# Kernel optimization log

Hardware: AMD Instinct MI355X
Metric: run time of the kernel (lower is better)

Reference implementation:

```python
import jax, jax.numpy as jnp
import numpy as np

S, B, D = 2048, 32, 1024  # seq_len, batch, in_dim; out_dim = 2*D

def setup_inputs() -> dict:
    key = jax.random.key(0)
    k1, k2, k3, k4 = jax.random.split(key, 4)
    return {
        "input": jax.random.normal(k1, (S, B, D), dtype=jnp.float32),
        "h": jax.random.normal(k2, (B, D), dtype=jnp.float32),
        "Wi": jax.random.normal(k3, (D, D), dtype=jnp.float32) * 0.02,
        "Wo": jax.random.normal(k4, (D, 2 * D), dtype=jnp.float32) * 0.02,
    }

def reference(input, h, Wi, Wo):
    # semi = Wi(h), broadcast over seq dim (torch expand_as)
    semi = h @ Wi.T                                   # [B, D]
    # score logits: elementwise mult + sum over feature dim
    logits = jnp.einsum('sbd,bd->bs', input, semi)    # [B, S]
    # legacy nn.Softmax() on 2D tensor normalizes over dim=1 (= seq)
    attn = jax.nn.softmax(logits, axis=1)             # [B, S]
    # weighted sum over sequence
    s_tilde = jnp.einsum('bs,sbd->bd', attn, input)   # [B, D]
    # output projection + tanh
    c_t = jnp.tanh(jnp.concatenate([s_tilde, h], axis=1) @ Wo.T)  # [B, D]
    return c_t
```

## Files before the change

kernel.cpp:

```cpp
#include <hip/hip_runtime.h>
#include <math.h>

#define S_LEN    2048
#define BATCH    32
#define DIM      1024
#define P_CHUNKS 32
#define CHUNK    (S_LEN / P_CHUNKS)
#define ROWS_PER_WAVE (CHUNK / 4)
#define NPART    (P_CHUNKS * 4)

__global__ __launch_bounds__(256) void gemm_skinny(
    const float* __restrict__ A, const float* __restrict__ W,
    float* __restrict__ out, int K, int Dout, int act)
{
    __shared__ __align__(16) float At[2][32 * 256];

    const int t    = threadIdx.x;
    const int lane = t & 63;
    const int wid  = t >> 6;
    const int d    = blockIdx.x * 4 + wid;

    float acc[32];
#pragma unroll
    for (int b = 0; b < 32; ++b) acc[b] = 0.0f;

    float4 sreg[8];
#pragma unroll
    for (int i = 0; i < 8; ++i) {
        int f4id = t + i * 256;
        int bb   = f4id >> 6;
        int c4   = f4id & 63;
        sreg[i] = ((const float4*)(A + (size_t)bb * K))[c4];
    }
    float4 w4 = ((const float4*)(W + (size_t)d * K))[lane];

    int buf = 0;
    for (int k0 = 0; k0 < K; k0 += 256) {
#pragma unroll
        for (int i = 0; i < 8; ++i) {
            int f4id = t + i * 256;
            int bb   = f4id >> 6;
            int c4   = f4id & 63;
            ((float4*)At[buf])[bb * 64 + c4] = sreg[i];
        }
        __syncthreads();

        float4 w4c = w4;
        if (k0 + 256 < K) {
            const int k1 = k0 + 256;
#pragma unroll
            for (int i = 0; i < 8; ++i) {
                int f4id = t + i * 256;
                int bb   = f4id >> 6;
                int c4   = f4id & 63;
                sreg[i] = ((const float4*)(A + (size_t)bb * K + k1))[c4];
            }
            w4 = ((const float4*)(W + (size_t)d * K + k1))[lane];
        }

#pragma unroll
        for (int b = 0; b < 32; ++b) {
            float4 a4 = ((const float4*)At[buf])[b * 64 + lane];
            acc[b] = fmaf(w4c.x, a4.x, acc[b]);
            acc[b] = fmaf(w4c.y, a4.y, acc[b]);
            acc[b] = fmaf(w4c.z, a4.z, acc[b]);
            acc[b] = fmaf(w4c.w, a4.w, acc[b]);
        }
        buf ^= 1;
    }

    float mine = 0.0f;
#pragma unroll
    for (int b = 0; b < 32; ++b) {
        float v = acc[b];
#pragma unroll
        for (int off = 32; off > 0; off >>= 1) v += __shfl_xor(v, off, 64);
        if (lane == b) mine = v;
    }
    if (lane < 32) {
        float o = act ? tanhf(mine) : mine;
        out[(size_t)lane * Dout + d] = o;
    }
}

__global__ __launch_bounds__(256) void attn_partial(
    const float* __restrict__ input, const float* __restrict__ semi,
    float* __restrict__ pacc, float* __restrict__ pm, float* __restrict__ pl)
{
    const int p    = blockIdx.x;
    const int b    = blockIdx.y;
    const int t    = threadIdx.x;
    const int lane = t & 63;
    const int w    = t >> 6;
    const int part = p * 4 + w;
    const int s0   = p * CHUNK + w * ROWS_PER_WAVE;

    const float4* sp = (const float4*)(semi + (size_t)b * DIM);
    const float4 sm0 = sp[lane];
    const float4 sm1 = sp[lane + 64];
    const float4 sm2 = sp[lane + 128];
    const float4 sm3 = sp[lane + 192];

    const float4* rp = (const float4*)(input + ((size_t)s0 * BATCH + b) * DIM);
    const size_t rstride = (size_t)BATCH * DIM / 4;

    float m = -INFINITY, l = 0.0f;
    float4 a0 = make_float4(0.f, 0.f, 0.f, 0.f);
    float4 a1 = a0, a2 = a0, a3 = a0;

    float4 x0 = rp[lane], x1 = rp[lane + 64], x2 = rp[lane + 128], x3 = rp[lane + 192];

#pragma unroll 1
    for (int j = 0; j < ROWS_PER_WAVE; ++j) {
        const float4 c0 = x0, c1 = x1, c2 = x2, c3 = x3;
        if (j + 1 < ROWS_PER_WAVE) {
            const float4* np = rp + (size_t)(j + 1) * rstride;
            x0 = np[lane];       x1 = np[lane + 64];
            x2 = np[lane + 128]; x3 = np[lane + 192];
        }

        float pd = c0.x * sm0.x;
        pd = fmaf(c0.y, sm0.y, pd); pd = fmaf(c0.z, sm0.z, pd); pd = fmaf(c0.w, sm0.w, pd);
        pd = fmaf(c1.x, sm1.x, pd); pd = fmaf(c1.y, sm1.y, pd);
        pd = fmaf(c1.z, sm1.z, pd); pd = fmaf(c1.w, sm1.w, pd);
        pd = fmaf(c2.x, sm2.x, pd); pd = fmaf(c2.y, sm2.y, pd);
        pd = fmaf(c2.z, sm2.z, pd); pd = fmaf(c2.w, sm2.w, pd);
        pd = fmaf(c3.x, sm3.x, pd); pd = fmaf(c3.y, sm3.y, pd);
        pd = fmaf(c3.z, sm3.z, pd); pd = fmaf(c3.w, sm3.w, pd);

#pragma unroll
        for (int off = 32; off > 0; off >>= 1) pd += __shfl_xor(pd, off, 64);

        const float mn = fmaxf(m, pd);
        const float sc = __expf(m - mn);
        const float f  = __expf(pd - mn);
        a0.x = fmaf(f, c0.x, a0.x * sc); a0.y = fmaf(f, c0.y, a0.y * sc);
        a0.z = fmaf(f, c0.z, a0.z * sc); a0.w = fmaf(f, c0.w, a0.w * sc);
        a1.x = fmaf(f, c1.x, a1.x * sc); a1.y = fmaf(f, c1.y, a1.y * sc);
        a1.z = fmaf(f, c1.z, a1.z * sc); a1.w = fmaf(f, c1.w, a1.w * sc);
        a2.x = fmaf(f, c2.x, a2.x * sc); a2.y = fmaf(f, c2.y, a2.y * sc);
        a2.z = fmaf(f, c2.z, a2.z * sc); a2.w = fmaf(f, c2.w, a2.w * sc);
        a3.x = fmaf(f, c3.x, a3.x * sc); a3.y = fmaf(f, c3.y, a3.y * sc);
        a3.z = fmaf(f, c3.z, a3.z * sc); a3.w = fmaf(f, c3.w, a3.w * sc);
        l = fmaf(l, sc, f);
        m = mn;
    }

    float4* op = (float4*)(pacc + ((size_t)b * NPART + part) * DIM);
    op[lane]       = a0;
    op[lane + 64]  = a1;
    op[lane + 128] = a2;
    op[lane + 192] = a3;
    if (lane == 0) {
        pm[b * NPART + part] = m;
        pl[b * NPART + part] = l;
    }
}

__global__ __launch_bounds__(256) void combine(
    const float* __restrict__ pacc, const float* __restrict__ pm,
    const float* __restrict__ pl, const float* __restrict__ h,
    float* __restrict__ cat)
{
    const int b = blockIdx.x;
    const int q = blockIdx.y;
    const int t = threadIdx.x;

    __shared__ float fsc[NPART];
    __shared__ float smv[NPART], slv[NPART];
    __shared__ float Linv;

    if (t < NPART) {
        smv[t] = pm[b * NPART + t];
        slv[t] = pl[b * NPART + t];
    }
    __syncthreads();

    if (t < 64) {
        const float m0 = smv[t], m1 = smv[t + 64];
        float mx = fmaxf(m0, m1);
#pragma unroll
        for (int off = 32; off > 0; off >>= 1) mx = fmaxf(mx, __shfl_xor(mx, off, 64));
        const float f0 = __expf(m0 - mx);
        const float f1 = __expf(m1 - mx);
        fsc[t]      = f0;
        fsc[t + 64] = f1;
        float L = fmaf(slv[t], f0, slv[t + 64] * f1);
#pragma unroll
        for (int off = 32; off > 0; off >>= 1) L += __shfl_xor(L, off, 64);
        if (t == 0) Linv = 1.0f / L;
    }
    __syncthreads();

    const int d = q * 256 + t;
    const float* pb = pacc + (size_t)b * NPART * DIM + d;
    float s0 = 0.f, s1 = 0.f, s2 = 0.f, s3 = 0.f;
#pragma unroll
    for (int pp = 0; pp < NPART; pp += 4) {
        s0 = fmaf(fsc[pp + 0], pb[(size_t)(pp + 0) * DIM], s0);
        s1 = fmaf(fsc[pp + 1], pb[(size_t)(pp + 1) * DIM], s1);
        s2 = fmaf(fsc[pp + 2], pb[(size_t)(pp + 2) * DIM], s2);
        s3 = fmaf(fsc[pp + 3], pb[(size_t)(pp + 3) * DIM], s3);
    }
    const float sum = (s0 + s1) + (s2 + s3);

    cat[(size_t)b * (2 * DIM) + d]       = sum * Linv;
    cat[(size_t)b * (2 * DIM) + DIM + d] = h[(size_t)b * DIM + d];
}

extern "C" void kernel_launch(void* const* d_in, const int* in_sizes, int n_in,
                              void* d_out, int out_size, void* d_ws, size_t ws_size,
                              hipStream_t stream)
{
    const float* input = (const float*)d_in[0];
    const float* h     = (const float*)d_in[1];
    const float* Wi    = (const float*)d_in[2];
    const float* Wo    = (const float*)d_in[3];
    float* out = (float*)d_out;

    float* ws   = (float*)d_ws;
    float* semi = ws;
    float* pacc = semi + 32 * 1024;
    float* pm   = pacc + (size_t)32 * NPART * 1024;
    float* pl   = pm + 32 * NPART;
    float* cat  = pl + 32 * NPART;

    hipLaunchKernelGGL(gemm_skinny, dim3(256), dim3(256), 0, stream,
                       h, Wi, semi, 1024, 1024, 0);
    hipLaunchKernelGGL(attn_partial, dim3(P_CHUNKS, BATCH), dim3(256), 0, stream,
                       input, semi, pacc, pm, pl);
    hipLaunchKernelGGL(combine, dim3(BATCH, 4), dim3(256), 0, stream,
                       pacc, pm, pl, h, cat);
    hipLaunchKernelGGL(gemm_skinny, dim3(256), dim3(256), 0, stream,
                       cat, Wo, out, 2048, 1024, 1);
}
```

Measured before the change: 415.8 us.

## Merge per-wave softmax partials in LDS and add lazy max rescaling

Each attention block now merges its four per-wave online-softmax partials through shared memory and writes one partial per block. This cuts the partial accumulator traffic and the combine kernel's reads by four. The online softmax also rescales the accumulators only when a new logit exceeds the running max by more than a threshold, which removes two exps and a multiply per element on most rows. The trade-offs are an extra block-level sync and LDS use, plus accumulators that can grow by up to e^8 before rescaling.

```diff
diff --git a/kernel.cpp b/kernel.cpp
--- a/kernel.cpp
+++ b/kernel.cpp
@@ -7,7 +7,6 @@
 #define P_CHUNKS 32
 #define CHUNK    (S_LEN / P_CHUNKS)
 #define ROWS_PER_WAVE (CHUNK / 4)
-#define NPART    (P_CHUNKS * 4)
 
 __global__ __launch_bounds__(256) void gemm_skinny(
     const float* __restrict__ A, const float* __restrict__ W,
@@ -92,8 +91,10 @@
     const int t    = threadIdx.x;
     const int lane = t & 63;
     const int w    = t >> 6;
-    const int part = p * 4 + w;
     const int s0   = p * CHUNK + w * ROWS_PER_WAVE;
+
+    __shared__ __align__(16) float accs[4][DIM];
+    __shared__ float smw[4], slw[4];
 
     const float4* sp = (const float4*)(semi + (size_t)b * DIM);
     const float4 sm0 = sp[lane];
@@ -126,34 +127,61 @@
         pd = fmaf(c2.x, sm2.x, pd); pd = fmaf(c2.y, sm2.y, pd);
         pd = fmaf(c2.z, sm2.z, pd); pd = fmaf(c2.w, sm2.w, pd);
         pd = fmaf(c3.x, sm3.x, pd); pd = fmaf(c3.y, sm3.y, pd);
-        pd = fmaf(c3.z, sm3.z, pd); pd = fmaf(c3.w, sm3.w, pd);
+        pd = fmaf(c3.w, sm3.w, pd); pd = fmaf(c3.z, sm3.z, pd);
 
 #pragma unroll
         for (int off = 32; off > 0; off >>= 1) pd += __shfl_xor(pd, off, 64);
 
-        const float mn = fmaxf(m, pd);
-        const float sc = __expf(m - mn);
-        const float f  = __expf(pd - mn);
-        a0.x = fmaf(f, c0.x, a0.x * sc); a0.y = fmaf(f, c0.y, a0.y * sc);
-        a0.z = fmaf(f, c0.z, a0.z * sc); a0.w = fmaf(f, c0.w, a0.w * sc);
-        a1.x = fmaf(f, c1.x, a1.x * sc); a1.y = fmaf(f, c1.y, a1.y * sc);
-        a1.z = fmaf(f, c1.z, a1.z * sc); a1.w = fmaf(f, c1.w, a1.w * sc);
-        a2.x = fmaf(f, c2.x, a2.x * sc); a2.y = fmaf(f, c2.y, a2.y * sc);
-        a2.z = fmaf(f, c2.z, a2.z * sc); a2.w = fmaf(f, c2.w, a2.w * sc);
-        a3.x = fmaf(f, c3.x, a3.x * sc); a3.y = fmaf(f, c3.y, a3.y * sc);
-        a3.z = fmaf(f, c3.z, a3.z * sc); a3.w = fmaf(f, c3.w, a3.w * sc);
-        l = fmaf(l, sc, f);
-        m = mn;
-    }
-
-    float4* op = (float4*)(pacc + ((size_t)b * NPART + part) * DIM);
-    op[lane]       = a0;
-    op[lane + 64]  = a1;
-    op[lane + 128] = a2;
-    op[lane + 192] = a3;
-    if (lane == 0) {
-        pm[b * NPART + part] = m;
-        pl[b * NPART + part] = l;
+        if (pd > m + 8.0f) {
+            const float sc = __expf(m - pd);
+            a0.x *= sc; a0.y *= sc; a0.z *= sc; a0.w *= sc;
+            a1.x *= sc; a1.y *= sc; a1.z *= sc; a1.w *= sc;
+            a2.x *= sc; a2.y *= sc; a2.z *= sc; a2.w *= sc;
+            a3.x *= sc; a3.y *= sc; a3.z *= sc; a3.w *= sc;
+            l *= sc;
+            m = pd;
+        }
+        const float f = __expf(pd - m);
+        a0.x = fmaf(f, c0.x, a0.x); a0.y = fmaf(f, c0.y, a0.y);
+        a0.z = fmaf(f, c0.z, a0.z); a0.w = fmaf(f, c0.w, a0.w);
+        a1.x = fmaf(f, c1.x, a1.x); a1.y = fmaf(f, c1.y, a1.y);
+        a1.z = fmaf(f, c1.z, a1.z); a1.w = fmaf(f, c1.w, a1.w);
+        a2.x = fmaf(f, c2.x, a2.x); a2.y = fmaf(f, c2.y, a2.y);
+        a2.z = fmaf(f, c2.z, a2.z); a2.w = fmaf(f, c2.w, a2.w);
+        a3.x = fmaf(f, c3.x, a3.x); a3.y = fmaf(f, c3.y, a3.y);
+        a3.z = fmaf(f, c3.z, a3.z); a3.w = fmaf(f, c3.w, a3.w);
+        l += f;
+    }
+
+    float4* as = (float4*)accs[w];
+    as[lane]       = a0;
+    as[lane + 64]  = a1;
+    as[lane + 128] = a2;
+    as[lane + 192] = a3;
+    if (lane == 0) { smw[w] = m; slw[w] = l; }
+    __syncthreads();
+
+    const float M  = fmaxf(fmaxf(smw[0], smw[1]), fmaxf(smw[2], smw[3]));
+    const float f0 = __expf(smw[0] - M);
+    const float f1 = __expf(smw[1] - M);
+    const float f2 = __expf(smw[2] - M);
+    const float f3 = __expf(smw[3] - M);
+
+    const float4 r0 = ((const float4*)accs[0])[t];
+    const float4 r1 = ((const float4*)accs[1])[t];
+    const float4 r2 = ((const float4*)accs[2])[t];
+    const float4 r3 = ((const float4*)accs[3])[t];
+    float4 o;
+    o.x = fmaf(f3, r3.x, fmaf(f2, r2.x, fmaf(f1, r1.x, f0 * r0.x)));
+    o.y = fmaf(f3, r3.y, fmaf(f2, r2.y, fmaf(f1, r1.y, f0 * r0.y)));
+    o.z = fmaf(f3, r3.z, fmaf(f2, r2.z, fmaf(f1, r1.z, f0 * r0.z)));
+    o.w = fmaf(f3, r3.w, fmaf(f2, r2.w, fmaf(f1, r1.w, f0 * r0.w)));
+
+    ((float4*)(pacc + ((size_t)b * P_CHUNKS + p) * DIM))[t] = o;
+    if (t == 0) {
+        pm[b * P_CHUNKS + p] = M;
+        pl[b * P_CHUNKS + p] =
+            fmaf(f3, slw[3], fmaf(f2, slw[2], fmaf(f1, slw[1], f0 * slw[0])));
     }
 }
 
@@ -166,37 +194,30 @@
     const int q = blockIdx.y;
     const int t = threadIdx.x;
 
-    __shared__ float fsc[NPART];
-    __shared__ float smv[NPART], slv[NPART];
+    __shared__ float fsc[P_CHUNKS];
     __shared__ float Linv;
 
-    if (t < NPART) {
-        smv[t] = pm[b * NPART + t];
-        slv[t] = pl[b * NPART + t];
+    if (t < 32) {
+        const float mv = pm[b * P_CHUNKS + t];
+        const float lv = pl[b * P_CHUNKS + t];
+        float mx = mv;
+#pragma unroll
+        for (int off = 16; off > 0; off >>= 1)
+            mx = fmaxf(mx, __shfl_xor(mx, off, 64));
+        const float f = __expf(mv - mx);
+        fsc[t] = f;
+        float L = lv * f;
+#pragma unroll
+        for (int off = 16; off > 0; off >>= 1) L += __shfl_xor(L, off, 64);
+        if (t == 0) Linv = 1.0f / L;
     }
     __syncthreads();
 
-    if (t < 64) {
-        const float m0 = smv[t], m1 = smv[t + 64];
-        float mx = fmaxf(m0, m1);
-#pragma unroll
-        for (int off = 32; off > 0; off >>= 1) mx = fmaxf(mx, __shfl_xor(mx, off, 64));
-        const float f0 = __expf(m0 - mx);
-        const float f1 = __expf(m1 - mx);
-        fsc[t]      = f0;
-        fsc[t + 64] = f1;
-        float L = fmaf(slv[t], f0, slv[t + 64] * f1);
-#pragma unroll
-        for (int off = 32; off > 0; off >>= 1) L += __shfl_xor(L, off, 64);
-        if (t == 0) Linv = 1.0f / L;
-    }
-    __syncthreads();
-
     const int d = q * 256 + t;
-    const float* pb = pacc + (size_t)b * NPART * DIM + d;
+    const float* pb = pacc + (size_t)b * P_CHUNKS * DIM + d;
     float s0 = 0.f, s1 = 0.f, s2 = 0.f, s3 = 0.f;
 #pragma unroll
-    for (int pp = 0; pp < NPART; pp += 4) {
+    for (int pp = 0; pp < P_CHUNKS; pp += 4) {
         s0 = fmaf(fsc[pp + 0], pb[(size_t)(pp + 0) * DIM], s0);
         s1 = fmaf(fsc[pp + 1], pb[(size_t)(pp + 1) * DIM], s1);
         s2 = fmaf(fsc[pp + 2], pb[(size_t)(pp + 2) * DIM], s2);
@@ -221,9 +242,9 @@
     float* ws   = (float*)d_ws;
     float* semi = ws;
     float* pacc = semi + 32 * 1024;
-    float* pm   = pacc + (size_t)32 * NPART * 1024;
-    float* pl   = pm + 32 * NPART;
-    float* cat  = pl + 32 * NPART;
+    float* pm   = pacc + (size_t)32 * P_CHUNKS * 1024;
+    float* pl   = pm + 32 * P_CHUNKS;
+    float* cat  = pl + 32 * P_CHUNKS;
 
     hipLaunchKernelGGL(gemm_skinny, dim3(256), dim3(256), 0, stream,
                        h, Wi, semi, 1024, 1024, 0);
```

Measured after the change: 413.8 us. About the same (-0.5%).
